# Kernel optimization log

Hardware: AMD Instinct MI355X
Metric: run time of the kernel (lower is better)

Reference implementation:

```python
import jax, jax.numpy as jnp
import numpy as np

K = 7  # local_kernel_size


def conv2d(x, w, b, pad):
    # x: [B,C,H,W], w: [O,I,kh,kw]
    y = jax.lax.conv_general_dilated(
        x, w, window_strides=(1, 1), padding=[(pad, pad), (pad, pad)],
        dimension_numbers=("NCHW", "OIHW", "NCHW"))
    return y + b[None, :, None, None]


def kernel_normalize(kernel, k):
    # kernel: [B, k*k, H, W]; zero-mean over tap dim, then add 1/(k*k)
    km = jnp.mean(kernel, axis=1, keepdims=True)
    return kernel - km + 1.0 / (k * k)


def local_conv_feat(img, kernel, k):
    # Fused dynamic local conv: avoids materializing [B,C,k*k,H,W].
    # Tap order matches F.unfold row-major (dy, dx).
    B, C, H, W = img.shape
    pad = (k - 1) // 2
    imgp = jnp.pad(img, ((0, 0), (0, 0), (pad, pad), (pad, pad)))
    out = jnp.zeros_like(img)
    for dy in range(k):
        for dx in range(k):
            idx = dy * k + dx
            out = out + imgp[:, :, dy:dy + H, dx:dx + W] * kernel[:, idx:idx + 1]
    return out


def setup_inputs() -> dict:
    key = jax.random.key(0)
    ks = jax.random.split(key, 14)
    B, C, H, W = 4, 64, 128, 128
    w = lambda k, shape: jax.random.normal(k, shape, jnp.float32) * 0.05
    return {
        "x": jax.random.normal(ks[0], (B, C, H, W), jnp.float32),
        "kernel_features": jax.random.normal(ks[1], (B, C, H, W), jnp.float32),
        # feature_path: two 3x3 convs
        "fw1": w(ks[2], (C, C, 3, 3)), "fb1": jnp.zeros((C,), jnp.float32),
        "fw2": w(ks[3], (C, C, 3, 3)), "fb2": jnp.zeros((C,), jnp.float32),
        # multiplicative_path: two 3x3 convs
        "mw1": w(ks[4], (C, C, 3, 3)), "mb1": jnp.zeros((C,), jnp.float32),
        "mw2": w(ks[5], (C, C, 3, 3)), "mb2": jnp.zeros((C,), jnp.float32),
        # local_filter_path: two 1x1 convs, last outputs k*k channels
        "lw1": w(ks[6], (C, C, 1, 1)), "lb1": jnp.zeros((C,), jnp.float32),
        "lw2": w(ks[7], (K * K, C, 1, 1)), "lb2": jnp.zeros((K * K,), jnp.float32),
    }


def reference(x, kernel_features, fw1, fb1, fw2, fb2, mw1, mb1, mw2, mb2, lw1, lb1, lw2, lb2):
    # feature_path: ReLU -> conv3x3 -> ReLU -> conv3x3
    fp = conv2d(jax.nn.relu(conv2d(jax.nn.relu(x), fw1, fb1, 1)), fw2, fb2, 1)
    # multiplicative_path: conv3x3 -> ReLU -> conv3x3
    mp = conv2d(jax.nn.relu(conv2d(kernel_features, mw1, mb1, 1)), mw2, mb2, 1)
    # local_filter_path: conv1x1 -> ReLU -> conv1x1 (-> k*k channels)
    lp = conv2d(jax.nn.relu(conv2d(kernel_features, lw1, lb1, 0)), lw2, lb2, 0)
    lp = kernel_normalize(lp, K)
    feat = fp * mp
    filtered = local_conv_feat(feat, lp, K)
    return x + filtered
```

## Files before the change

### kernel.cpp

```cpp
#include <hip/hip_runtime.h>
#include <hip/hip_bf16.h>

#define Cc 64
#define Hc 128
#define Wc 128
#define HWc (Hc * Wc)
#define Bc 4

typedef __attribute__((ext_vector_type(8))) short short8;
typedef __attribute__((ext_vector_type(4))) float float4v;

static __device__ __forceinline__ unsigned short f2bu(float f) {
    __hip_bfloat16 h = __float2bfloat16(f);
    return *(unsigned short*)&h;
}
static __device__ __forceinline__ float bulo(unsigned int u) {
    return __uint_as_float((u & 0xffffu) << 16);
}
static __device__ __forceinline__ float buhi(unsigned int u) {
    return __uint_as_float(u & 0xffff0000u);
}

static __device__ __forceinline__ void gl_lds16(const void* g, void* l) {
    __builtin_amdgcn_global_load_lds(
        (const __attribute__((address_space(1))) unsigned int*)g,
        (__attribute__((address_space(3))) unsigned int*)l, 16, 0, 0);
}

__global__ __launch_bounds__(256) void prep_k(
    const float* __restrict__ x, const float* __restrict__ kf,
    const float* __restrict__ fw1, const float* __restrict__ fw2,
    const float* __restrict__ mw1, const float* __restrict__ mw2,
    const float* __restrict__ lw1, const float* __restrict__ lw2,
    unsigned short* __restrict__ xb, unsigned short* __restrict__ kfb,
    unsigned short* __restrict__ wbase, unsigned short* __restrict__ zpage)
{
    const int bid = blockIdx.x;
    const int tid = threadIdx.x;

    if (bid < 512) {
        const bool isx = bid < 256;
        const float* src = isx ? x : kf;
        unsigned short* dst = isx ? xb : kfb;
        const int px = (isx ? bid : bid - 256) * 256 + tid;
        const int b  = px >> 14;
        const int hw = px & 16383;
        const float* s = src + (size_t)b * Cc * HWc + hw;
        unsigned short* d = dst + (size_t)px * Cc;
#pragma unroll
        for (int c8 = 0; c8 < 8; ++c8) {
            unsigned int pk[4];
#pragma unroll
            for (int jp = 0; jp < 4; ++jp) {
                float v0 = s[(size_t)(c8 * 8 + jp * 2 + 0) * HWc];
                float v1 = s[(size_t)(c8 * 8 + jp * 2 + 1) * HWc];
                if (isx) { v0 = fmaxf(v0, 0.f); v1 = fmaxf(v1, 0.f); }
                pk[jp] = (unsigned int)f2bu(v0) | ((unsigned int)f2bu(v1) << 16);
            }
            *(uint4*)(d + c8 * 8) = make_uint4(pk[0], pk[1], pk[2], pk[3]);
        }
    } else if (bid < 584) {
        const int wbid  = bid - 512;
        const int which = wbid / 18;
        const float* w = (which == 0) ? fw1 : (which == 1) ? fw2 : (which == 2) ? mw1 : mw2;
        unsigned short* wb = wbase + (size_t)which * 36864;
        const int g = (wbid % 18) * 256 + tid;
        if (g >= 4608) return;
        const int lane = g & 63;
        const int smt  = g >> 6;
        const int s    = smt >> 2;
        const int mt   = smt & 3;
        const int co   = mt * 16 + (lane & 15);
        const int kb   = s * 32 + (lane >> 4) * 8;
        unsigned int pk[4];
#pragma unroll
        for (int jp = 0; jp < 4; ++jp) {
            int k0 = kb + jp * 2, k1 = k0 + 1;
            float v0 = w[((size_t)co * Cc + (k0 & 63)) * 9 + (k0 >> 6)];
            float v1 = w[((size_t)co * Cc + (k1 & 63)) * 9 + (k1 >> 6)];
            pk[jp] = (unsigned int)f2bu(v0) | ((unsigned int)f2bu(v1) << 16);
        }
        *(uint4*)(wb + (size_t)g * 8) = make_uint4(pk[0], pk[1], pk[2], pk[3]);
    } else if (bid < 588) {
        const int wbid  = bid - 584;
        const int which = wbid >> 1;
        const float* w = which ? lw2 : lw1;
        const int Cout = which ? 49 : 64;
        unsigned short* wb = wbase + 4 * 36864 + (size_t)which * 4096;
        const int g = (wbid & 1) * 256 + tid;
        const int lane = g & 63;
        const int smt  = g >> 6;
        const int s    = smt >> 2;
        const int mt   = smt & 3;
        const int co   = mt * 16 + (lane & 15);
        const int kb   = s * 32 + (lane >> 4) * 8;
        unsigned int pk[4];
#pragma unroll
        for (int jp = 0; jp < 4; ++jp) {
            int k0 = kb + jp * 2, k1 = k0 + 1;
            float v0 = (co < Cout) ? w[(size_t)co * Cc + k0] : 0.f;
            float v1 = (co < Cout) ? w[(size_t)co * Cc + k1] : 0.f;
            pk[jp] = (unsigned int)f2bu(v0) | ((unsigned int)f2bu(v1) << 16);
        }
        *(uint4*)(wb + (size_t)g * 8) = make_uint4(pk[0], pk[1], pk[2], pk[3]);
    } else {
        if (tid < 64) ((unsigned int*)zpage)[tid] = 0;
    }
}

#define STAGE_DMA(INPTR, SBUF)                                                \
    for (int k = wv; k < 33; k += 4) {                                        \
        const int u_  = k * 8 + (lane >> 3);                                  \
        const int j_  = lane & 7;                                             \
        const int r_  = u_ / 66;                                              \
        const int c_  = u_ - r_ * 66;                                         \
        const int gh_ = h0 - 1 + r_;                                          \
        const int gw_ = w0 - 1 + c_;                                          \
        const bool ok_ = ((unsigned)gh_ < (unsigned)Hc) && ((unsigned)gw_ < (unsigned)Wc); \
        const int ch_ = j_ ^ (u_ & 7);                                        \
        const unsigned short* g_ = ok_                                        \
            ? (INPTR) + ((((size_t)b * Hc + gh_) * Wc + gw_) << 6) + (ch_ << 3) \
            : zpage + (ch_ << 3);                                             \
        gl_lds16(g_, &(SBUF)[k * 512]);                                       \
    }

#define LOAD_A(W, s, m) (*(const short8*)((W) + (size_t)(s) * 2048 + (size_t)(m) * 512))
#define LOAD_B(SB, s, nt) ({                                                  \
        const int tap_ = (s) >> 1;                                            \
        const int qb_  = rowb[tap_ / 3] + tap_ % 3;                           \
        const int ch0_ = ((s) & 1) * 4 + quad;                                \
        *(const short8*)&(SB)[(qb_ + (nt) * 16) * 64 + ((ch0_ ^ (qb_ & 7)) << 3)]; })

#define CONV_GEMM(APTR, ACC, SB)                                              \
    {                                                                         \
        short8 a_buf[4][2], b_cur[4], b_nxt[4];                               \
        _Pragma("unroll")                                                     \
        for (int q = 0; q < 3; ++q)                                           \
            _Pragma("unroll")                                                 \
            for (int m = 0; m < 2; ++m) a_buf[q][m] = LOAD_A(APTR, q, m);     \
        _Pragma("unroll")                                                     \
        for (int nt = 0; nt < 4; ++nt) b_cur[nt] = LOAD_B(SB, 0, nt);         \
        _Pragma("unroll")                                                     \
        for (int s = 0; s < 18; ++s) {                                        \
            if (s + 3 < 18) {                                                 \
                _Pragma("unroll")                                             \
                for (int m = 0; m < 2; ++m)                                   \
                    a_buf[(s + 3) & 3][m] = LOAD_A(APTR, s + 3, m);           \
            }                                                                 \
            if (s + 1 < 18) {                                                 \
                _Pragma("unroll")                                             \
                for (int nt = 0; nt < 4; ++nt)                                \
                    b_nxt[nt] = LOAD_B(SB, s + 1, nt);                        \
            }                                                                 \
            _Pragma("unroll")                                                 \
            for (int nt = 0; nt < 4; ++nt)                                    \
                _Pragma("unroll")                                             \
                for (int m = 0; m < 2; ++m)                                   \
                    ACC[m][nt] = __builtin_amdgcn_mfma_f32_16x16x32_bf16(     \
                        a_buf[s & 3][m], b_cur[nt], ACC[m][nt], 0, 0, 0);     \
            if (s + 1 < 18) {                                                 \
                _Pragma("unroll")                                             \
                for (int nt = 0; nt < 4; ++nt) b_cur[nt] = b_nxt[nt];         \
            }                                                                 \
        }                                                                     \
    }

__global__ __launch_bounds__(256) void conv1_lp_k(
    const unsigned short* __restrict__ in0,
    const unsigned short* __restrict__ in1,
    const unsigned short* __restrict__ wfrag0,
    const unsigned short* __restrict__ wfrag1,
    const float* __restrict__ bias0,
    const float* __restrict__ bias1,
    const unsigned short* __restrict__ zpage,
    unsigned short* __restrict__ out0,
    unsigned short* __restrict__ out1,
    const unsigned short* __restrict__ w1, const float* __restrict__ b1,
    const unsigned short* __restrict__ w2, const float* __restrict__ b2,
    unsigned short* __restrict__ lpout)
{
    __shared__ unsigned short s_b[264 * 64];

    const int tid  = threadIdx.x;
    const int lane = tid & 63;
    const int wv   = tid >> 6;
    const int quad = lane >> 4;
    const int glin = blockIdx.x;
    const int xcd  = glin & 7;
    const int slot = glin >> 3;

    if (slot < 128) {
        const int sel = slot >> 6;
        const int hti = slot & 63;
        const int b   = xcd >> 1;
        const int w0  = (xcd & 1) * 64;
        const int h0  = hti * 2;

        const unsigned short* in    = sel ? in1 : in0;
        const unsigned short* wfrag = sel ? wfrag1 : wfrag0;
        const float*          bias  = sel ? bias1 : bias0;
        unsigned short*       out   = sel ? out1 : out0;

        STAGE_DMA(in, s_b);
        __syncthreads();

        const int rowsel = wv >> 1;
        const int cohalf = wv & 1;
        const int n15    = lane & 15;
        const unsigned short* aptr = wfrag + (((size_t)(cohalf * 2) * 64 + lane) << 3);

        int rowb[3];
#pragma unroll
        for (int ky = 0; ky < 3; ++ky) rowb[ky] = (rowsel + ky) * 66 + n15;

        float4v acc[2][4];
#pragma unroll
        for (int m = 0; m < 2; ++m)
#pragma unroll
            for (int nt = 0; nt < 4; ++nt) acc[m][nt] = (float4v){0.f, 0.f, 0.f, 0.f};

        CONV_GEMM(aptr, acc, s_b);

        const int h = h0 + rowsel;
#pragma unroll
        for (int m = 0; m < 2; ++m) {
            const int mt  = cohalf * 2 + m;
            const int co0 = mt * 16 + quad * 4;
            float4 bv = *(const float4*)&bias[co0];
#pragma unroll
            for (int nt = 0; nt < 4; ++nt) {
                const size_t pix = ((size_t)b * Hc + h) * Wc + w0 + nt * 16 + n15;
                ushort4 pk;
                pk.x = f2bu(fmaxf(acc[m][nt][0] + bv.x, 0.f));
                pk.y = f2bu(fmaxf(acc[m][nt][1] + bv.y, 0.f));
                pk.z = f2bu(fmaxf(acc[m][nt][2] + bv.z, 0.f));
                pk.w = f2bu(fmaxf(acc[m][nt][3] + bv.w, 0.f));
                *(ushort4*)&out[pix * Cc + co0] = pk;
            }
        }
    } else {
        const int lpid = xcd * 128 + (slot - 128);
        const int p    = lane & 15;
        const size_t pix = (size_t)lpid * 64 + wv * 16 + p;
        unsigned short* st = &s_b[wv * 1024];

        float4v acc1[4];
#pragma unroll
        for (int mt = 0; mt < 4; ++mt) acc1[mt] = (float4v){0.f, 0.f, 0.f, 0.f};
#pragma unroll
        for (int s = 0; s < 2; ++s) {
            short8 bfr = *(const short8*)&in1[pix * Cc + s * 32 + quad * 8];
#pragma unroll
            for (int mt = 0; mt < 4; ++mt) {
                short8 afr = *(const short8*)&w1[(size_t)(((s * 4 + mt) << 6) + lane) << 3];
                acc1[mt] = __builtin_amdgcn_mfma_f32_16x16x32_bf16(afr, bfr, acc1[mt], 0, 0, 0);
            }
        }

#pragma unroll
        for (int mt = 0; mt < 4; ++mt) {
            const int co0 = mt * 16 + quad * 4;
            float4 bv = *(const float4*)&b1[co0];
            ushort4 pk;
            pk.x = f2bu(fmaxf(acc1[mt][0] + bv.x, 0.f));
            pk.y = f2bu(fmaxf(acc1[mt][1] + bv.y, 0.f));
            pk.z = f2bu(fmaxf(acc1[mt][2] + bv.z, 0.f));
            pk.w = f2bu(fmaxf(acc1[mt][3] + bv.w, 0.f));
            const int cg = co0 >> 3;
            *(ushort4*)&st[p * 64 + ((cg ^ (p & 7)) << 3) + (quad & 1) * 4] = pk;
        }
        __syncthreads();

        float4v acc2[4];
#pragma unroll
        for (int mt = 0; mt < 4; ++mt) acc2[mt] = (float4v){0.f, 0.f, 0.f, 0.f};
#pragma unroll
        for (int s = 0; s < 2; ++s) {
            const int cg = s * 4 + quad;
            short8 bfr = *(const short8*)&st[p * 64 + ((cg ^ (p & 7)) << 3)];
#pragma unroll
            for (int mt = 0; mt < 4; ++mt) {
                short8 afr = *(const short8*)&w2[(size_t)(((s * 4 + mt) << 6) + lane) << 3];
                acc2[mt] = __builtin_amdgcn_mfma_f32_16x16x32_bf16(afr, bfr, acc2[mt], 0, 0, 0);
            }
        }

        float v[4][4];
        float partial = 0.f;
#pragma unroll
        for (int mt = 0; mt < 4; ++mt) {
#pragma unroll
            for (int r = 0; r < 4; ++r) {
                const int tap = mt * 16 + quad * 4 + r;
                float val = (tap < 49) ? (acc2[mt][r] + b2[tap]) : 0.f;
                v[mt][r] = val;
                partial += val;
            }
        }
        partial += __shfl_xor(partial, 16, 64);
        partial += __shfl_xor(partial, 32, 64);
        const float m = partial * (1.f / 49.f) - (1.f / 49.f);

        const int b  = (int)(pix >> 14);
        const int hw = (int)(pix & 16383);
#pragma unroll
        for (int mt = 0; mt < 4; ++mt) {
#pragma unroll
            for (int r = 0; r < 4; ++r) {
                const int tap = mt * 16 + quad * 4 + r;
                if (tap < 49)
                    lpout[((size_t)b * 49 + tap) * HWc + hw] = f2bu(v[mt][r] - m);
            }
        }
    }
}

__global__ __launch_bounds__(256) void conv2_fused_k(
    const unsigned short* __restrict__ t1f,
    const unsigned short* __restrict__ t1m,
    const unsigned short* __restrict__ wf,
    const unsigned short* __restrict__ wm,
    const float* __restrict__ bf,
    const float* __restrict__ bm,
    const unsigned short* __restrict__ zpage,
    unsigned short* __restrict__ featp)
{
    __shared__ unsigned short s_b2[2][264 * 64];

    const int tid  = threadIdx.x;
    const int lane = tid & 63;
    const int wv   = tid >> 6;
    const int glin = blockIdx.x;
    const int xcd  = glin & 7;
    const int slot = glin >> 3;
    const int b    = xcd >> 1;
    const int w0   = (xcd & 1) * 64;
    const int h0   = slot * 2;

    STAGE_DMA(t1f, s_b2[0]);
    STAGE_DMA(t1m, s_b2[1]);
    __syncthreads();

    const int rowsel = wv >> 1;
    const int cohalf = wv & 1;
    const int quad   = lane >> 4;
    const int n15    = lane & 15;

    int rowb[3];
#pragma unroll
    for (int ky = 0; ky < 3; ++ky) rowb[ky] = (rowsel + ky) * 66 + n15;

    float4v acc[2][4];
#pragma unroll
    for (int m = 0; m < 2; ++m)
#pragma unroll
        for (int nt = 0; nt < 4; ++nt) acc[m][nt] = (float4v){0.f, 0.f, 0.f, 0.f};

    {
        const unsigned short* aptr = wf + (((size_t)(cohalf * 2) * 64 + lane) << 3);
        CONV_GEMM(aptr, acc, s_b2[0]);
    }

    float fpv[2][4][4];
#pragma unroll
    for (int m = 0; m < 2; ++m) {
        const int mt  = cohalf * 2 + m;
        const int co0 = mt * 16 + quad * 4;
        float4 bv = *(const float4*)&bf[co0];
#pragma unroll
        for (int nt = 0; nt < 4; ++nt) {
            fpv[m][nt][0] = bulo((unsigned int)f2bu(acc[m][nt][0] + bv.x));
            fpv[m][nt][1] = bulo((unsigned int)f2bu(acc[m][nt][1] + bv.y));
            fpv[m][nt][2] = bulo((unsigned int)f2bu(acc[m][nt][2] + bv.z));
            fpv[m][nt][3] = bulo((unsigned int)f2bu(acc[m][nt][3] + bv.w));
        }
    }

#pragma unroll
    for (int m = 0; m < 2; ++m)
#pragma unroll
        for (int nt = 0; nt < 4; ++nt) acc[m][nt] = (float4v){0.f, 0.f, 0.f, 0.f};

    {
        const unsigned short* aptr = wm + (((size_t)(cohalf * 2) * 64 + lane) << 3);
        CONV_GEMM(aptr, acc, s_b2[1]);
    }

    const int h = h0 + rowsel;
#pragma unroll
    for (int m = 0; m < 2; ++m) {
        const int mt  = cohalf * 2 + m;
        const int co0 = mt * 16 + quad * 4;
        float4 bv = *(const float4*)&bm[co0];
#pragma unroll
        for (int nt = 0; nt < 4; ++nt) {
            const int px = h * Wc + w0 + nt * 16 + n15;
            float v[4] = {acc[m][nt][0] + bv.x, acc[m][nt][1] + bv.y,
                          acc[m][nt][2] + bv.z, acc[m][nt][3] + bv.w};
#pragma unroll
            for (int r = 0; r < 4; ++r)
                featp[((size_t)b * Cc + co0 + r) * HWc + px] =
                    f2bu(v[r] * fpv[m][nt][r]);
        }
    }
}

__global__ __launch_bounds__(256) void local_conv_v4(
    const float* __restrict__ x, const unsigned short* __restrict__ featp,
    const unsigned short* __restrict__ lp, float* __restrict__ out)
{
    const int tid  = threadIdx.x;
    const int glin = blockIdx.x;
    const int xcd  = glin & 7;
    const int slot = glin >> 3;
    const int pair = xcd * 8 + (slot >> 4);
    const int cg   = slot & 15;
    const int b    = pair >> 4;
    const int hti  = pair & 15;

    const int w4  = (tid & 31) * 4;
    const int ro  = tid >> 5;
    const int h   = hti * 8 + ro;
    const int c0  = cg * 4;

    float msk[12];
#pragma unroll
    for (int e = 0; e < 12; ++e) {
        int gw = w4 - 4 + e;
        msk[e] = ((unsigned)gw < (unsigned)Wc) ? 1.f : 0.f;
    }

    float acc[4][4];
#pragma unroll
    for (int ch = 0; ch < 4; ++ch)
#pragma unroll
        for (int p = 0; p < 4; ++p) acc[ch][p] = 0.f;

    const unsigned short* lpb = lp + (size_t)b * 49 * HWc + (size_t)h * Wc + w4;
    const unsigned short* fb  = featp + ((size_t)b * Cc + c0) * HWc;

#pragma unroll
    for (int dy = 0; dy < 7; ++dy) {
        const int gh = h + dy - 3;
        if ((unsigned)gh >= (unsigned)Hc) continue;

        float lpf[7][4];
#pragma unroll
        for (int dx = 0; dx < 7; ++dx) {
            uint2 lv = *(const uint2*)&lpb[(size_t)(dy * 7 + dx) * HWc];
            lpf[dx][0] = bulo(lv.x); lpf[dx][1] = buhi(lv.x);
            lpf[dx][2] = bulo(lv.y); lpf[dx][3] = buhi(lv.y);
        }

        const unsigned short* frow = fb + (size_t)gh * Wc + w4;
#pragma unroll
        for (int ch = 0; ch < 4; ++ch) {
            const unsigned short* fr = frow + (size_t)ch * HWc;
            uint2 a  = *(const uint2*)(fr - 4);
            uint2 bq = *(const uint2*)(fr);
            uint2 cq = *(const uint2*)(fr + 4);
            float f[12];
            f[0]  = bulo(a.x);             f[1]  = buhi(a.x) * msk[1];
            f[2]  = bulo(a.y) * msk[2];    f[3]  = buhi(a.y) * msk[3];
            f[4]  = bulo(bq.x);            f[5]  = buhi(bq.x);
            f[6]  = bulo(bq.y);            f[7]  = buhi(bq.y);
            f[8]  = bulo(cq.x) * msk[8];   f[9]  = buhi(cq.x) * msk[9];
            f[10] = bulo(cq.y) * msk[10];  f[11] = buhi(cq.y);
#pragma unroll
            for (int dx = 0; dx < 7; ++dx)
#pragma unroll
                for (int p = 0; p < 4; ++p)
                    acc[ch][p] = fmaf(f[p + dx + 1], lpf[dx][p], acc[ch][p]);
        }
    }

#pragma unroll
    for (int ch = 0; ch < 4; ++ch) {
        const size_t idx = ((size_t)b * Cc + c0 + ch) * HWc + (size_t)h * Wc + w4;
        float4 xv = *(const float4*)&x[idx];
        float4 r  = {acc[ch][0] + xv.x, acc[ch][1] + xv.y,
                     acc[ch][2] + xv.z, acc[ch][3] + xv.w};
        *(float4*)&out[idx] = r;
    }
}

extern "C" void kernel_launch(void* const* d_in, const int* in_sizes, int n_in,
                              void* d_out, int out_size, void* d_ws, size_t ws_size,
                              hipStream_t stream)
{
    const float* x   = (const float*)d_in[0];
    const float* kf  = (const float*)d_in[1];
    const float* fw1 = (const float*)d_in[2];
    const float* fb1 = (const float*)d_in[3];
    const float* fw2 = (const float*)d_in[4];
    const float* fb2 = (const float*)d_in[5];
    const float* mw1 = (const float*)d_in[6];
    const float* mb1 = (const float*)d_in[7];
    const float* mw2 = (const float*)d_in[8];
    const float* mb2 = (const float*)d_in[9];
    const float* lw1 = (const float*)d_in[10];
    const float* lb1 = (const float*)d_in[11];
    const float* lw2 = (const float*)d_in[12];
    const float* lb2 = (const float*)d_in[13];

    float* out = (float*)d_out;
    char*  ws  = (char*)d_ws;

    const size_t NBH = (size_t)Bc * HWc * Cc * 2;
    const size_t LPH = (size_t)Bc * 49 * HWc * 2;
    const size_t WBA = (size_t)(4 * 36864 + 2 * 4096) * 2;

    unsigned short* t1f   = (unsigned short*)(ws);
    unsigned short* t1m   = (unsigned short*)(ws + NBH);
    unsigned short* featp = (unsigned short*)(ws + 2 * NBH);
    unsigned short* lpb   = (unsigned short*)(ws + 3 * NBH);
    unsigned short* xb    = (unsigned short*)(ws + 3 * NBH + LPH);
    unsigned short* kfb   = (unsigned short*)((char*)xb + NBH);
    unsigned short* wbase = (unsigned short*)((char*)kfb + NBH);
    unsigned short* zpage = (unsigned short*)((char*)wbase + WBA);
    unsigned short* wb1   = wbase;
    unsigned short* wb2   = wbase + 36864;
    unsigned short* wb3   = wbase + 2 * 36864;
    unsigned short* wb4   = wbase + 3 * 36864;
    unsigned short* wl1   = wbase + 4 * 36864;
    unsigned short* wl2   = wbase + 4 * 36864 + 4096;

    dim3 blk(256);

    prep_k<<<dim3(589), blk, 0, stream>>>(x, kf, fw1, fw2, mw1, mw2, lw1, lw2,
                                          xb, kfb, wbase, zpage);

    conv1_lp_k<<<dim3(2048), blk, 0, stream>>>(xb, kfb, wb1, wb3, fb1, mb1, zpage,
                                               t1f, t1m, wl1, lb1, wl2, lb2, lpb);

    conv2_fused_k<<<dim3(512), blk, 0, stream>>>(t1f, t1m, wb2, wb4, fb2, mb2,
                                                 zpage, featp);

    local_conv_v4<<<dim3(1024), blk, 0, stream>>>(x, featp, lpb, out);
}
```

Baseline: 161.6 us.

## Replace LDS-staged 3x3 conv GEMMs with direct global-load implicit GEMM

Removes the global_load_lds staging of a halo tile into shared memory for both 3x3 conv stages. Each wave now reads its B fragments for one output row straight from global/L2, with edge pixels redirected to an enlarged zero page. Each block covers one row instead of two, and all four output-channel tiles move into one wave. The conv2 grid doubles and launch bounds request 3 blocks per SM. This drops the LDS barrier and its footprint, but loses LDS reuse of overlapping taps and leans on the cache for nine-fold redundant activation reads.

```diff
diff --git a/kernel.cpp b/kernel.cpp
--- a/kernel.cpp
+++ b/kernel.cpp
@@ -19,12 +19,6 @@
 }
 static __device__ __forceinline__ float buhi(unsigned int u) {
     return __uint_as_float(u & 0xffff0000u);
-}
-
-static __device__ __forceinline__ void gl_lds16(const void* g, void* l) {
-    __builtin_amdgcn_global_load_lds(
-        (const __attribute__((address_space(1))) unsigned int*)g,
-        (__attribute__((address_space(3))) unsigned int*)l, 16, 0, 0);
 }
 
 __global__ __launch_bounds__(256) void prep_k(
@@ -104,155 +98,129 @@
         }
         *(uint4*)(wb + (size_t)g * 8) = make_uint4(pk[0], pk[1], pk[2], pk[3]);
     } else {
-        if (tid < 64) ((unsigned int*)zpage)[tid] = 0;
-    }
-}
-
-#define STAGE_DMA(INPTR, SBUF)                                                \
-    for (int k = wv; k < 33; k += 4) {                                        \
-        const int u_  = k * 8 + (lane >> 3);                                  \
-        const int j_  = lane & 7;                                             \
-        const int r_  = u_ / 66;                                              \
-        const int c_  = u_ - r_ * 66;                                         \
-        const int gh_ = h0 - 1 + r_;                                          \
-        const int gw_ = w0 - 1 + c_;                                          \
-        const bool ok_ = ((unsigned)gh_ < (unsigned)Hc) && ((unsigned)gw_ < (unsigned)Wc); \
-        const int ch_ = j_ ^ (u_ & 7);                                        \
-        const unsigned short* g_ = ok_                                        \
-            ? (INPTR) + ((((size_t)b * Hc + gh_) * Wc + gw_) << 6) + (ch_ << 3) \
-            : zpage + (ch_ << 3);                                             \
-        gl_lds16(g_, &(SBUF)[k * 512]);                                       \
-    }
-
-#define LOAD_A(W, s, m) (*(const short8*)((W) + (size_t)(s) * 2048 + (size_t)(m) * 512))
-#define LOAD_B(SB, s, nt) ({                                                  \
-        const int tap_ = (s) >> 1;                                            \
-        const int qb_  = rowb[tap_ / 3] + tap_ % 3;                           \
-        const int ch0_ = ((s) & 1) * 4 + quad;                                \
-        *(const short8*)&(SB)[(qb_ + (nt) * 16) * 64 + ((ch0_ ^ (qb_ & 7)) << 3)]; })
-
-#define CONV_GEMM(APTR, ACC, SB)                                              \
+        uint4 z = make_uint4(0u, 0u, 0u, 0u);
+        ((uint4*)zpage)[tid] = z;
+        ((uint4*)zpage)[256 + tid] = z;
+    }
+}
+
+static __device__ __forceinline__ void conv_gemm_direct(
+    const unsigned short* __restrict__ src,
+    const unsigned short* __restrict__ wsrc,
+    const unsigned short* __restrict__ zp,
+    int b, int h, int w0, int wv, int lane, float4v acc[4])
+{
+    const int n15  = lane & 15;
+    const int quad = lane >> 4;
+    const int laneoff = n15 * 64 + quad * 8;
+    const unsigned short* zb = zp + laneoff;
+    const bool eL = (w0 == 0)  && (wv == 0) && (n15 == 0);
+    const bool eR = (w0 == 64) && (wv == 3) && (n15 == 15);
+
+    const unsigned short* base[3];
+    const unsigned short* baseL[3];
+    const unsigned short* baseR[3];
+#pragma unroll
+    for (int ky = 0; ky < 3; ++ky) {
+        const int gh = h - 1 + ky;
+        const unsigned short* p = ((unsigned)gh < (unsigned)Hc)
+            ? src + (size_t)((b * Hc + gh) * Wc) * 64
+                  + (w0 - 1 + wv * 16) * 64 + laneoff
+            : zb;
+        base[ky]  = p;
+        baseL[ky] = eL ? zb : p;
+        baseR[ky] = eR ? zb : p;
+    }
+
+#pragma unroll
+    for (int s = 0; s < 18; ++s) {
+        const int tap = s >> 1;
+        const int sh  = s & 1;
+        const int ky  = tap / 3;
+        const int kx  = tap % 3;
+        const unsigned short* bp =
+            (kx == 0) ? baseL[ky] : (kx == 2) ? baseR[ky] : base[ky];
+        short8 bf = *(const short8*)(bp + kx * 64 + sh * 32);
+#pragma unroll
+        for (int mt = 0; mt < 4; ++mt) {
+            short8 af = *(const short8*)(wsrc + (size_t)s * 2048 + mt * 512 + lane * 8);
+            acc[mt] = __builtin_amdgcn_mfma_f32_16x16x32_bf16(af, bf, acc[mt], 0, 0, 0);
+        }
+    }
+}
+
+#define CONV_EPI_NHWC(ACC, BIASP, OUTP, RELU)                                 \
     {                                                                         \
-        short8 a_buf[4][2], b_cur[4], b_nxt[4];                               \
+        const int wpix_ = w0 + wv * 16 + n15;                                 \
+        const size_t pb_ = (((size_t)b * Hc + h) * Wc + wpix_) * Cc;          \
         _Pragma("unroll")                                                     \
-        for (int q = 0; q < 3; ++q)                                           \
-            _Pragma("unroll")                                                 \
-            for (int m = 0; m < 2; ++m) a_buf[q][m] = LOAD_A(APTR, q, m);     \
-        _Pragma("unroll")                                                     \
-        for (int nt = 0; nt < 4; ++nt) b_cur[nt] = LOAD_B(SB, 0, nt);         \
-        _Pragma("unroll")                                                     \
-        for (int s = 0; s < 18; ++s) {                                        \
-            if (s + 3 < 18) {                                                 \
-                _Pragma("unroll")                                             \
-                for (int m = 0; m < 2; ++m)                                   \
-                    a_buf[(s + 3) & 3][m] = LOAD_A(APTR, s + 3, m);           \
-            }                                                                 \
-            if (s + 1 < 18) {                                                 \
-                _Pragma("unroll")                                             \
-                for (int nt = 0; nt < 4; ++nt)                                \
-                    b_nxt[nt] = LOAD_B(SB, s + 1, nt);                        \
-            }                                                                 \
-            _Pragma("unroll")                                                 \
-            for (int nt = 0; nt < 4; ++nt)                                    \
-                _Pragma("unroll")                                             \
-                for (int m = 0; m < 2; ++m)                                   \
-                    ACC[m][nt] = __builtin_amdgcn_mfma_f32_16x16x32_bf16(     \
-                        a_buf[s & 3][m], b_cur[nt], ACC[m][nt], 0, 0, 0);     \
-            if (s + 1 < 18) {                                                 \
-                _Pragma("unroll")                                             \
-                for (int nt = 0; nt < 4; ++nt) b_cur[nt] = b_nxt[nt];         \
-            }                                                                 \
+        for (int mt = 0; mt < 4; ++mt) {                                      \
+            const int co0_ = mt * 16 + quad * 4;                              \
+            float4 bv_ = *(const float4*)&(BIASP)[co0_];                      \
+            float r0 = (ACC)[mt][0] + bv_.x, r1 = (ACC)[mt][1] + bv_.y;       \
+            float r2 = (ACC)[mt][2] + bv_.z, r3 = (ACC)[mt][3] + bv_.w;       \
+            if (RELU) { r0 = fmaxf(r0, 0.f); r1 = fmaxf(r1, 0.f);             \
+                        r2 = fmaxf(r2, 0.f); r3 = fmaxf(r3, 0.f); }           \
+            ushort4 pk_;                                                      \
+            pk_.x = f2bu(r0); pk_.y = f2bu(r1);                               \
+            pk_.z = f2bu(r2); pk_.w = f2bu(r3);                               \
+            *(ushort4*)&(OUTP)[pb_ + co0_] = pk_;                             \
         }                                                                     \
     }
 
-__global__ __launch_bounds__(256) void conv1_lp_k(
-    const unsigned short* __restrict__ in0,
-    const unsigned short* __restrict__ in1,
-    const unsigned short* __restrict__ wfrag0,
-    const unsigned short* __restrict__ wfrag1,
-    const float* __restrict__ bias0,
-    const float* __restrict__ bias1,
+__global__ __launch_bounds__(256, 3) void conv1_direct_k(
+    const unsigned short* __restrict__ xb,
+    const unsigned short* __restrict__ kfb,
+    const unsigned short* __restrict__ wb1,
+    const unsigned short* __restrict__ wb3,
+    const float* __restrict__ fb1, const float* __restrict__ mb1,
+    const unsigned short* __restrict__ wl1, const float* __restrict__ lb1,
+    const unsigned short* __restrict__ wl2, const float* __restrict__ lb2,
     const unsigned short* __restrict__ zpage,
-    unsigned short* __restrict__ out0,
-    unsigned short* __restrict__ out1,
-    const unsigned short* __restrict__ w1, const float* __restrict__ b1,
-    const unsigned short* __restrict__ w2, const float* __restrict__ b2,
-    unsigned short* __restrict__ lpout)
-{
-    __shared__ unsigned short s_b[264 * 64];
+    unsigned short* __restrict__ t1f, unsigned short* __restrict__ t1m,
+    unsigned short* __restrict__ lpb)
+{
+    __shared__ unsigned short s_lp[4 * 1024];
 
     const int tid  = threadIdx.x;
     const int lane = tid & 63;
     const int wv   = tid >> 6;
     const int quad = lane >> 4;
+    const int n15  = lane & 15;
     const int glin = blockIdx.x;
     const int xcd  = glin & 7;
     const int slot = glin >> 3;
 
     if (slot < 128) {
-        const int sel = slot >> 6;
-        const int hti = slot & 63;
-        const int b   = xcd >> 1;
-        const int w0  = (xcd & 1) * 64;
-        const int h0  = hti * 2;
-
-        const unsigned short* in    = sel ? in1 : in0;
-        const unsigned short* wfrag = sel ? wfrag1 : wfrag0;
-        const float*          bias  = sel ? bias1 : bias0;
-        unsigned short*       out   = sel ? out1 : out0;
-
-        STAGE_DMA(in, s_b);
-        __syncthreads();
-
-        const int rowsel = wv >> 1;
-        const int cohalf = wv & 1;
-        const int n15    = lane & 15;
-        const unsigned short* aptr = wfrag + (((size_t)(cohalf * 2) * 64 + lane) << 3);
-
-        int rowb[3];
-#pragma unroll
-        for (int ky = 0; ky < 3; ++ky) rowb[ky] = (rowsel + ky) * 66 + n15;
-
-        float4v acc[2][4];
-#pragma unroll
-        for (int m = 0; m < 2; ++m)
-#pragma unroll
-            for (int nt = 0; nt < 4; ++nt) acc[m][nt] = (float4v){0.f, 0.f, 0.f, 0.f};
-
-        CONV_GEMM(aptr, acc, s_b);
-
-        const int h = h0 + rowsel;
-#pragma unroll
-        for (int m = 0; m < 2; ++m) {
-            const int mt  = cohalf * 2 + m;
-            const int co0 = mt * 16 + quad * 4;
-            float4 bv = *(const float4*)&bias[co0];
-#pragma unroll
-            for (int nt = 0; nt < 4; ++nt) {
-                const size_t pix = ((size_t)b * Hc + h) * Wc + w0 + nt * 16 + n15;
-                ushort4 pk;
-                pk.x = f2bu(fmaxf(acc[m][nt][0] + bv.x, 0.f));
-                pk.y = f2bu(fmaxf(acc[m][nt][1] + bv.y, 0.f));
-                pk.z = f2bu(fmaxf(acc[m][nt][2] + bv.z, 0.f));
-                pk.w = f2bu(fmaxf(acc[m][nt][3] + bv.w, 0.f));
-                *(ushort4*)&out[pix * Cc + co0] = pk;
-            }
-        }
+        const int b  = xcd >> 1;
+        const int w0 = (xcd & 1) * 64;
+        const int h  = slot;
+
+        float4v acc[4];
+#pragma unroll
+        for (int mt = 0; mt < 4; ++mt) acc[mt] = (float4v){0.f, 0.f, 0.f, 0.f};
+        conv_gemm_direct(xb, wb1, zpage, b, h, w0, wv, lane, acc);
+        CONV_EPI_NHWC(acc, fb1, t1f, true);
+
+#pragma unroll
+        for (int mt = 0; mt < 4; ++mt) acc[mt] = (float4v){0.f, 0.f, 0.f, 0.f};
+        conv_gemm_direct(kfb, wb3, zpage, b, h, w0, wv, lane, acc);
+        CONV_EPI_NHWC(acc, mb1, t1m, true);
     } else {
         const int lpid = xcd * 128 + (slot - 128);
         const int p    = lane & 15;
         const size_t pix = (size_t)lpid * 64 + wv * 16 + p;
-        unsigned short* st = &s_b[wv * 1024];
+        unsigned short* st = &s_lp[wv * 1024];
 
         float4v acc1[4];
 #pragma unroll
         for (int mt = 0; mt < 4; ++mt) acc1[mt] = (float4v){0.f, 0.f, 0.f, 0.f};
 #pragma unroll
         for (int s = 0; s < 2; ++s) {
-            short8 bfr = *(const short8*)&in1[pix * Cc + s * 32 + quad * 8];
+            short8 bfr = *(const short8*)&kfb[pix * Cc + s * 32 + quad * 8];
 #pragma unroll
             for (int mt = 0; mt < 4; ++mt) {
-                short8 afr = *(const short8*)&w1[(size_t)(((s * 4 + mt) << 6) + lane) << 3];
+                short8 afr = *(const short8*)&wl1[(size_t)(((s * 4 + mt) << 6) + lane) << 3];
                 acc1[mt] = __builtin_amdgcn_mfma_f32_16x16x32_bf16(afr, bfr, acc1[mt], 0, 0, 0);
             }
         }
@@ -260,7 +228,7 @@
 #pragma unroll
         for (int mt = 0; mt < 4; ++mt) {
             const int co0 = mt * 16 + quad * 4;
-            float4 bv = *(const float4*)&b1[co0];
+            float4 bv = *(const float4*)&lb1[co0];
             ushort4 pk;
             pk.x = f2bu(fmaxf(acc1[mt][0] + bv.x, 0.f));
             pk.y = f2bu(fmaxf(acc1[mt][1] + bv.y, 0.f));
@@ -280,7 +248,7 @@
             short8 bfr = *(const short8*)&st[p * 64 + ((cg ^ (p & 7)) << 3)];
 #pragma unroll
             for (int mt = 0; mt < 4; ++mt) {
-                short8 afr = *(const short8*)&w2[(size_t)(((s * 4 + mt) << 6) + lane) << 3];
+                short8 afr = *(const short8*)&wl2[(size_t)(((s * 4 + mt) << 6) + lane) << 3];
                 acc2[mt] = __builtin_amdgcn_mfma_f32_16x16x32_bf16(afr, bfr, acc2[mt], 0, 0, 0);
             }
         }
@@ -292,7 +260,7 @@
 #pragma unroll
             for (int r = 0; r < 4; ++r) {
                 const int tap = mt * 16 + quad * 4 + r;
-                float val = (tap < 49) ? (acc2[mt][r] + b2[tap]) : 0.f;
+                float val = (tap < 49) ? (acc2[mt][r] + lb2[tap]) : 0.f;
                 v[mt][r] = val;
                 partial += val;
             }
@@ -301,7 +269,7 @@
         partial += __shfl_xor(partial, 32, 64);
         const float m = partial * (1.f / 49.f) - (1.f / 49.f);
 
-        const int b  = (int)(pix >> 14);
+        const int bI = (int)(pix >> 14);
         const int hw = (int)(pix & 16383);
 #pragma unroll
         for (int mt = 0; mt < 4; ++mt) {
@@ -309,99 +277,64 @@
             for (int r = 0; r < 4; ++r) {
                 const int tap = mt * 16 + quad * 4 + r;
                 if (tap < 49)
-                    lpout[((size_t)b * 49 + tap) * HWc + hw] = f2bu(v[mt][r] - m);
+                    lpb[((size_t)bI * 49 + tap) * HWc + hw] = f2bu(v[mt][r] - m);
             }
         }
     }
 }
 
-__global__ __launch_bounds__(256) void conv2_fused_k(
+__global__ __launch_bounds__(256, 3) void conv2_direct_k(
     const unsigned short* __restrict__ t1f,
     const unsigned short* __restrict__ t1m,
-    const unsigned short* __restrict__ wf,
-    const unsigned short* __restrict__ wm,
-    const float* __restrict__ bf,
-    const float* __restrict__ bm,
+    const unsigned short* __restrict__ wb2,
+    const unsigned short* __restrict__ wb4,
+    const float* __restrict__ fb2, const float* __restrict__ mb2,
     const unsigned short* __restrict__ zpage,
     unsigned short* __restrict__ featp)
 {
-    __shared__ unsigned short s_b2[2][264 * 64];
-
     const int tid  = threadIdx.x;
     const int lane = tid & 63;
     const int wv   = tid >> 6;
+    const int quad = lane >> 4;
+    const int n15  = lane & 15;
     const int glin = blockIdx.x;
     const int xcd  = glin & 7;
-    const int slot = glin >> 3;
     const int b    = xcd >> 1;
     const int w0   = (xcd & 1) * 64;
-    const int h0   = slot * 2;
-
-    STAGE_DMA(t1f, s_b2[0]);
-    STAGE_DMA(t1m, s_b2[1]);
-    __syncthreads();
-
-    const int rowsel = wv >> 1;
-    const int cohalf = wv & 1;
-    const int quad   = lane >> 4;
-    const int n15    = lane & 15;
-
-    int rowb[3];
-#pragma unroll
-    for (int ky = 0; ky < 3; ++ky) rowb[ky] = (rowsel + ky) * 66 + n15;
-
-    float4v acc[2][4];
-#pragma unroll
-    for (int m = 0; m < 2; ++m)
-#pragma unroll
-        for (int nt = 0; nt < 4; ++nt) acc[m][nt] = (float4v){0.f, 0.f, 0.f, 0.f};
-
-    {
-        const unsigned short* aptr = wf + (((size_t)(cohalf * 2) * 64 + lane) << 3);
-        CONV_GEMM(aptr, acc, s_b2[0]);
-    }
-
-    float fpv[2][4][4];
-#pragma unroll
-    for (int m = 0; m < 2; ++m) {
-        const int mt  = cohalf * 2 + m;
+    const int h    = glin >> 3;
+
+    float4v acc[4];
+#pragma unroll
+    for (int mt = 0; mt < 4; ++mt) acc[mt] = (float4v){0.f, 0.f, 0.f, 0.f};
+    conv_gemm_direct(t1f, wb2, zpage, b, h, w0, wv, lane, acc);
+
+    float fpv[4][4];
+#pragma unroll
+    for (int mt = 0; mt < 4; ++mt) {
         const int co0 = mt * 16 + quad * 4;
-        float4 bv = *(const float4*)&bf[co0];
-#pragma unroll
-        for (int nt = 0; nt < 4; ++nt) {
-            fpv[m][nt][0] = bulo((unsigned int)f2bu(acc[m][nt][0] + bv.x));
-            fpv[m][nt][1] = bulo((unsigned int)f2bu(acc[m][nt][1] + bv.y));
-            fpv[m][nt][2] = bulo((unsigned int)f2bu(acc[m][nt][2] + bv.z));
-            fpv[m][nt][3] = bulo((unsigned int)f2bu(acc[m][nt][3] + bv.w));
-        }
-    }
-
-#pragma unroll
-    for (int m = 0; m < 2; ++m)
-#pragma unroll
-        for (int nt = 0; nt < 4; ++nt) acc[m][nt] = (float4v){0.f, 0.f, 0.f, 0.f};
-
-    {
-        const unsigned short* aptr = wm + (((size_t)(cohalf * 2) * 64 + lane) << 3);
-        CONV_GEMM(aptr, acc, s_b2[1]);
-    }
-
-    const int h = h0 + rowsel;
-#pragma unroll
-    for (int m = 0; m < 2; ++m) {
-        const int mt  = cohalf * 2 + m;
+        float4 bv = *(const float4*)&fb2[co0];
+        fpv[mt][0] = bulo((unsigned int)f2bu(acc[mt][0] + bv.x));
+        fpv[mt][1] = bulo((unsigned int)f2bu(acc[mt][1] + bv.y));
+        fpv[mt][2] = bulo((unsigned int)f2bu(acc[mt][2] + bv.z));
+        fpv[mt][3] = bulo((unsigned int)f2bu(acc[mt][3] + bv.w));
+    }
+
+#pragma unroll
+    for (int mt = 0; mt < 4; ++mt) acc[mt] = (float4v){0.f, 0.f, 0.f, 0.f};
+    conv_gemm_direct(t1m, wb4, zpage, b, h, w0, wv, lane, acc);
+
+    const int wpix = w0 + wv * 16 + n15;
+    const int px   = h * Wc + wpix;
+#pragma unroll
+    for (int mt = 0; mt < 4; ++mt) {
         const int co0 = mt * 16 + quad * 4;
-        float4 bv = *(const float4*)&bm[co0];
-#pragma unroll
-        for (int nt = 0; nt < 4; ++nt) {
-            const int px = h * Wc + w0 + nt * 16 + n15;
-            float v[4] = {acc[m][nt][0] + bv.x, acc[m][nt][1] + bv.y,
-                          acc[m][nt][2] + bv.z, acc[m][nt][3] + bv.w};
-#pragma unroll
-            for (int r = 0; r < 4; ++r)
-                featp[((size_t)b * Cc + co0 + r) * HWc + px] =
-                    f2bu(v[r] * fpv[m][nt][r]);
-        }
+        float4 bv = *(const float4*)&mb2[co0];
+        float v[4] = {acc[mt][0] + bv.x, acc[mt][1] + bv.y,
+                      acc[mt][2] + bv.z, acc[mt][3] + bv.w};
+#pragma unroll
+        for (int r = 0; r < 4; ++r)
+            featp[((size_t)b * Cc + co0 + r) * HWc + px] =
+                f2bu(v[r] * fpv[mt][r]);
     }
 }
 
@@ -530,11 +463,12 @@
     prep_k<<<dim3(589), blk, 0, stream>>>(x, kf, fw1, fw2, mw1, mw2, lw1, lw2,
                                           xb, kfb, wbase, zpage);
 
-    conv1_lp_k<<<dim3(2048), blk, 0, stream>>>(xb, kfb, wb1, wb3, fb1, mb1, zpage,
-                                               t1f, t1m, wl1, lb1, wl2, lb2, lpb);
-
-    conv2_fused_k<<<dim3(512), blk, 0, stream>>>(t1f, t1m, wb2, wb4, fb2, mb2,
-                                                 zpage, featp);
+    conv1_direct_k<<<dim3(2048), blk, 0, stream>>>(xb, kfb, wb1, wb3, fb1, mb1,
+                                                   wl1, lb1, wl2, lb2, zpage,
+                                                   t1f, t1m, lpb);
+
+    conv2_direct_k<<<dim3(1024), blk, 0, stream>>>(t1f, t1m, wb2, wb4, fb2, mb2,
+                                                   zpage, featp);
 
     local_conv_v4<<<dim3(1024), blk, 0, stream>>>(x, featp, lpb, out);
 }
```

Measured after the change: 207.4 us. 28.3% more time.

## Tile 3x3 convs by one output row per block instead of two

Applied to the files above, without the earlier changes.

The conv kernels now tile one output row per block instead of two. Each wave computes one 16-channel M tile rather than two, and grids grow to 3072 and 1024 blocks. The input halo staged in LDS shrinks from 4 to 3 rows, which halves per-wave accumulators and raises block count and occupancy. In exchange, halo reuse drops (3 rows staged per output row vs 2), so global and LDS traffic rises, and each wave issues half the MFMAs per weight fragment load.

```diff
diff --git a/kernel.cpp b/kernel.cpp
--- a/kernel.cpp
+++ b/kernel.cpp
@@ -108,15 +108,16 @@
     }
 }
 
-#define STAGE_DMA(INPTR, SBUF)                                                \
-    for (int k = wv; k < 33; k += 4) {                                        \
+#define STAGE_DMA3(INPTR, SBUF)                                               \
+    for (int k = wv; k < 25; k += 4) {                                        \
         const int u_  = k * 8 + (lane >> 3);                                  \
         const int j_  = lane & 7;                                             \
         const int r_  = u_ / 66;                                              \
         const int c_  = u_ - r_ * 66;                                         \
-        const int gh_ = h0 - 1 + r_;                                          \
+        const int gh_ = h - 1 + r_;                                           \
         const int gw_ = w0 - 1 + c_;                                          \
-        const bool ok_ = ((unsigned)gh_ < (unsigned)Hc) && ((unsigned)gw_ < (unsigned)Wc); \
+        const bool ok_ = (u_ < 198) &&                                        \
+            ((unsigned)gh_ < (unsigned)Hc) && ((unsigned)gw_ < (unsigned)Wc); \
         const int ch_ = j_ ^ (u_ & 7);                                        \
         const unsigned short* g_ = ok_                                        \
             ? (INPTR) + ((((size_t)b * Hc + gh_) * Wc + gw_) << 6) + (ch_ << 3) \
@@ -124,29 +125,23 @@
         gl_lds16(g_, &(SBUF)[k * 512]);                                       \
     }
 
-#define LOAD_A(W, s, m) (*(const short8*)((W) + (size_t)(s) * 2048 + (size_t)(m) * 512))
+#define LOAD_A1(W, s) (*(const short8*)((W) + (size_t)(s) * 2048))
 #define LOAD_B(SB, s, nt) ({                                                  \
         const int tap_ = (s) >> 1;                                            \
         const int qb_  = rowb[tap_ / 3] + tap_ % 3;                           \
         const int ch0_ = ((s) & 1) * 4 + quad;                                \
         *(const short8*)&(SB)[(qb_ + (nt) * 16) * 64 + ((ch0_ ^ (qb_ & 7)) << 3)]; })
 
-#define CONV_GEMM(APTR, ACC, SB)                                              \
+#define CONV_GEMM1(APTR, ACC, SB)                                             \
     {                                                                         \
-        short8 a_buf[4][2], b_cur[4], b_nxt[4];                               \
+        short8 a_buf[4], b_cur[4], b_nxt[4];                                  \
         _Pragma("unroll")                                                     \
-        for (int q = 0; q < 3; ++q)                                           \
-            _Pragma("unroll")                                                 \
-            for (int m = 0; m < 2; ++m) a_buf[q][m] = LOAD_A(APTR, q, m);     \
+        for (int q = 0; q < 3; ++q) a_buf[q] = LOAD_A1(APTR, q);              \
         _Pragma("unroll")                                                     \
         for (int nt = 0; nt < 4; ++nt) b_cur[nt] = LOAD_B(SB, 0, nt);         \
         _Pragma("unroll")                                                     \
         for (int s = 0; s < 18; ++s) {                                        \
-            if (s + 3 < 18) {                                                 \
-                _Pragma("unroll")                                             \
-                for (int m = 0; m < 2; ++m)                                   \
-                    a_buf[(s + 3) & 3][m] = LOAD_A(APTR, s + 3, m);           \
-            }                                                                 \
+            if (s + 3 < 18) a_buf[(s + 3) & 3] = LOAD_A1(APTR, s + 3);        \
             if (s + 1 < 18) {                                                 \
                 _Pragma("unroll")                                             \
                 for (int nt = 0; nt < 4; ++nt)                                \
@@ -154,10 +149,8 @@
             }                                                                 \
             _Pragma("unroll")                                                 \
             for (int nt = 0; nt < 4; ++nt)                                    \
-                _Pragma("unroll")                                             \
-                for (int m = 0; m < 2; ++m)                                   \
-                    ACC[m][nt] = __builtin_amdgcn_mfma_f32_16x16x32_bf16(     \
-                        a_buf[s & 3][m], b_cur[nt], ACC[m][nt], 0, 0, 0);     \
+                ACC[nt] = __builtin_amdgcn_mfma_f32_16x16x32_bf16(            \
+                    a_buf[s & 3], b_cur[nt], ACC[nt], 0, 0, 0);               \
             if (s + 1 < 18) {                                                 \
                 _Pragma("unroll")                                             \
                 for (int nt = 0; nt < 4; ++nt) b_cur[nt] = b_nxt[nt];         \
@@ -179,7 +172,7 @@
     const unsigned short* __restrict__ w2, const float* __restrict__ b2,
     unsigned short* __restrict__ lpout)
 {
-    __shared__ unsigned short s_b[264 * 64];
+    __shared__ unsigned short s_b[200 * 64];
 
     const int tid  = threadIdx.x;
     const int lane = tid & 63;
@@ -189,57 +182,48 @@
     const int xcd  = glin & 7;
     const int slot = glin >> 3;
 
-    if (slot < 128) {
-        const int sel = slot >> 6;
-        const int hti = slot & 63;
+    if (slot < 256) {
+        const int sel = slot >> 7;
+        const int h   = slot & 127;
         const int b   = xcd >> 1;
         const int w0  = (xcd & 1) * 64;
-        const int h0  = hti * 2;
 
         const unsigned short* in    = sel ? in1 : in0;
         const unsigned short* wfrag = sel ? wfrag1 : wfrag0;
         const float*          bias  = sel ? bias1 : bias0;
         unsigned short*       out   = sel ? out1 : out0;
 
-        STAGE_DMA(in, s_b);
+        STAGE_DMA3(in, s_b);
         __syncthreads();
 
-        const int rowsel = wv >> 1;
-        const int cohalf = wv & 1;
-        const int n15    = lane & 15;
-        const unsigned short* aptr = wfrag + (((size_t)(cohalf * 2) * 64 + lane) << 3);
+        const int n15 = lane & 15;
+        const unsigned short* aptr = wfrag + (((size_t)wv * 64 + lane) << 3);
 
         int rowb[3];
 #pragma unroll
-        for (int ky = 0; ky < 3; ++ky) rowb[ky] = (rowsel + ky) * 66 + n15;
-
-        float4v acc[2][4];
-#pragma unroll
-        for (int m = 0; m < 2; ++m)
-#pragma unroll
-            for (int nt = 0; nt < 4; ++nt) acc[m][nt] = (float4v){0.f, 0.f, 0.f, 0.f};
-
-        CONV_GEMM(aptr, acc, s_b);
-
-        const int h = h0 + rowsel;
-#pragma unroll
-        for (int m = 0; m < 2; ++m) {
-            const int mt  = cohalf * 2 + m;
-            const int co0 = mt * 16 + quad * 4;
-            float4 bv = *(const float4*)&bias[co0];
-#pragma unroll
-            for (int nt = 0; nt < 4; ++nt) {
-                const size_t pix = ((size_t)b * Hc + h) * Wc + w0 + nt * 16 + n15;
-                ushort4 pk;
-                pk.x = f2bu(fmaxf(acc[m][nt][0] + bv.x, 0.f));
-                pk.y = f2bu(fmaxf(acc[m][nt][1] + bv.y, 0.f));
-                pk.z = f2bu(fmaxf(acc[m][nt][2] + bv.z, 0.f));
-                pk.w = f2bu(fmaxf(acc[m][nt][3] + bv.w, 0.f));
-                *(ushort4*)&out[pix * Cc + co0] = pk;
-            }
+        for (int ky = 0; ky < 3; ++ky) rowb[ky] = ky * 66 + n15;
+
+        float4v acc[4];
+#pragma unroll
+        for (int nt = 0; nt < 4; ++nt) acc[nt] = (float4v){0.f, 0.f, 0.f, 0.f};
+
+        CONV_GEMM1(aptr, acc, s_b);
+
+        const int co0 = wv * 16 + quad * 4;
+        float4 bv = *(const float4*)&bias[co0];
+        const size_t rowbase = ((size_t)b * Hc + h) * Wc + w0;
+#pragma unroll
+        for (int nt = 0; nt < 4; ++nt) {
+            const size_t pix = rowbase + nt * 16 + n15;
+            ushort4 pk;
+            pk.x = f2bu(fmaxf(acc[nt][0] + bv.x, 0.f));
+            pk.y = f2bu(fmaxf(acc[nt][1] + bv.y, 0.f));
+            pk.z = f2bu(fmaxf(acc[nt][2] + bv.z, 0.f));
+            pk.w = f2bu(fmaxf(acc[nt][3] + bv.w, 0.f));
+            *(ushort4*)&out[pix * Cc + co0] = pk;
         }
     } else {
-        const int lpid = xcd * 128 + (slot - 128);
+        const int lpid = xcd * 128 + (slot - 256);
         const int p    = lane & 15;
         const size_t pix = (size_t)lpid * 64 + wv * 16 + p;
         unsigned short* st = &s_b[wv * 1024];
@@ -325,82 +309,68 @@
     const unsigned short* __restrict__ zpage,
     unsigned short* __restrict__ featp)
 {
-    __shared__ unsigned short s_b2[2][264 * 64];
+    __shared__ unsigned short s_b2[2][200 * 64];
 
     const int tid  = threadIdx.x;
     const int lane = tid & 63;
     const int wv   = tid >> 6;
     const int glin = blockIdx.x;
     const int xcd  = glin & 7;
-    const int slot = glin >> 3;
+    const int h    = glin >> 3;
     const int b    = xcd >> 1;
     const int w0   = (xcd & 1) * 64;
-    const int h0   = slot * 2;
-
-    STAGE_DMA(t1f, s_b2[0]);
-    STAGE_DMA(t1m, s_b2[1]);
+
+    STAGE_DMA3(t1f, s_b2[0]);
+    STAGE_DMA3(t1m, s_b2[1]);
     __syncthreads();
 
-    const int rowsel = wv >> 1;
-    const int cohalf = wv & 1;
-    const int quad   = lane >> 4;
-    const int n15    = lane & 15;
+    const int quad = lane >> 4;
+    const int n15  = lane & 15;
 
     int rowb[3];
 #pragma unroll
-    for (int ky = 0; ky < 3; ++ky) rowb[ky] = (rowsel + ky) * 66 + n15;
-
-    float4v acc[2][4];
-#pragma unroll
-    for (int m = 0; m < 2; ++m)
-#pragma unroll
-        for (int nt = 0; nt < 4; ++nt) acc[m][nt] = (float4v){0.f, 0.f, 0.f, 0.f};
-
+    for (int ky = 0; ky < 3; ++ky) rowb[ky] = ky * 66 + n15;
+
+    const int co0 = wv * 16 + quad * 4;
+
+    float4v acc[4];
+#pragma unroll
+    for (int nt = 0; nt < 4; ++nt) acc[nt] = (float4v){0.f, 0.f, 0.f, 0.f};
     {
-        const unsigned short* aptr = wf + (((size_t)(cohalf * 2) * 64 + lane) << 3);
-        CONV_GEMM(aptr, acc, s_b2[0]);
-    }
-
-    float fpv[2][4][4];
-#pragma unroll
-    for (int m = 0; m < 2; ++m) {
-        const int mt  = cohalf * 2 + m;
-        const int co0 = mt * 16 + quad * 4;
+        const unsigned short* aptr = wf + (((size_t)wv * 64 + lane) << 3);
+        CONV_GEMM1(aptr, acc, s_b2[0]);
+    }
+
+    float fpv[4][4];
+    {
         float4 bv = *(const float4*)&bf[co0];
 #pragma unroll
         for (int nt = 0; nt < 4; ++nt) {
-            fpv[m][nt][0] = bulo((unsigned int)f2bu(acc[m][nt][0] + bv.x));
-            fpv[m][nt][1] = bulo((unsigned int)f2bu(acc[m][nt][1] + bv.y));
-            fpv[m][nt][2] = bulo((unsigned int)f2bu(acc[m][nt][2] + bv.z));
-            fpv[m][nt][3] = bulo((unsigned int)f2bu(acc[m][nt][3] + bv.w));
-        }
-    }
-
-#pragma unroll
-    for (int m = 0; m < 2; ++m)
-#pragma unroll
-        for (int nt = 0; nt < 4; ++nt) acc[m][nt] = (float4v){0.f, 0.f, 0.f, 0.f};
-
+            fpv[nt][0] = bulo((unsigned int)f2bu(acc[nt][0] + bv.x));
+            fpv[nt][1] = bulo((unsigned int)f2bu(acc[nt][1] + bv.y));
+            fpv[nt][2] = bulo((unsigned int)f2bu(acc[nt][2] + bv.z));
+            fpv[nt][3] = bulo((unsigned int)f2bu(acc[nt][3] + bv.w));
+        }
+    }
+
+#pragma unroll
+    for (int nt = 0; nt < 4; ++nt) acc[nt] = (float4v){0.f, 0.f, 0.f, 0.f};
     {
-        const unsigned short* aptr = wm + (((size_t)(cohalf * 2) * 64 + lane) << 3);
-        CONV_GEMM(aptr, acc, s_b2[1]);
-    }
-
-    const int h = h0 + rowsel;
-#pragma unroll
-    for (int m = 0; m < 2; ++m) {
-        const int mt  = cohalf * 2 + m;
-        const int co0 = mt * 16 + quad * 4;
+        const unsigned short* aptr = wm + (((size_t)wv * 64 + lane) << 3);
+        CONV_GEMM1(aptr, acc, s_b2[1]);
+    }
+
+    {
         float4 bv = *(const float4*)&bm[co0];
 #pragma unroll
         for (int nt = 0; nt < 4; ++nt) {
             const int px = h * Wc + w0 + nt * 16 + n15;
-            float v[4] = {acc[m][nt][0] + bv.x, acc[m][nt][1] + bv.y,
-                          acc[m][nt][2] + bv.z, acc[m][nt][3] + bv.w};
+            float v[4] = {acc[nt][0] + bv.x, acc[nt][1] + bv.y,
+                          acc[nt][2] + bv.z, acc[nt][3] + bv.w};
 #pragma unroll
             for (int r = 0; r < 4; ++r)
                 featp[((size_t)b * Cc + co0 + r) * HWc + px] =
-                    f2bu(v[r] * fpv[m][nt][r]);
+                    f2bu(v[r] * fpv[nt][r]);
         }
     }
 }
@@ -530,11 +500,11 @@
     prep_k<<<dim3(589), blk, 0, stream>>>(x, kf, fw1, fw2, mw1, mw2, lw1, lw2,
                                           xb, kfb, wbase, zpage);
 
-    conv1_lp_k<<<dim3(2048), blk, 0, stream>>>(xb, kfb, wb1, wb3, fb1, mb1, zpage,
+    conv1_lp_k<<<dim3(3072), blk, 0, stream>>>(xb, kfb, wb1, wb3, fb1, mb1, zpage,
                                                t1f, t1m, wl1, lb1, wl2, lb2, lpb);
 
-    conv2_fused_k<<<dim3(512), blk, 0, stream>>>(t1f, t1m, wb2, wb4, fb2, mb2,
-                                                 zpage, featp);
+    conv2_fused_k<<<dim3(1024), blk, 0, stream>>>(t1f, t1m, wb2, wb4, fb2, mb2,
+                                                  zpage, featp);
 
     local_conv_v4<<<dim3(1024), blk, 0, stream>>>(x, featp, lpb, out);
 }
```

After: 164.7 us. No clear change (+1.9%).
